# Performance work log

Measured on AMD Instinct MI355X. Metric: run time of the kernel, lower is better.

Reference implementation:

```python
import jax, jax.numpy as jnp
import numpy as np

NUM_CLASSES = 100


def setup_inputs() -> dict:
    key = jax.random.key(0)
    k1, k2, k3, k4 = jax.random.split(key, 4)
    x = jax.random.normal(k1, (256, 2048), dtype=jnp.float32)
    W_model = jax.random.normal(k2, (2048, 64), dtype=jnp.float32)
    database_code = jax.random.normal(k3, (100000, 64), dtype=jnp.float32)
    database_labels = jax.random.randint(k4, (100000,), 0, NUM_CLASSES, dtype=jnp.int64)
    return {
        "x": x,
        "W_model": W_model,
        "database_code": database_code,
        "database_labels": database_labels,
        "K": 1000,
    }


def reference(x, W_model, database_code, database_labels, K):
    # model(x): single linear projection to hash-code space [B, d]
    out = x @ W_model
    # sim_score = out @ codes.T * -0.5 + num_classes/2  -> [B, N]
    sim = jnp.matmul(out, database_code.T) * -0.5 + NUM_CLASSES / 2
    # np.argpartition(sim, K)[:, :K] selects the K SMALLEST scores.
    # Equivalent set via top_k on negated scores.
    _, topk_idx = jax.lax.top_k(-sim, K)            # [B, K]
    topk_labels = database_labels[topk_idx]          # [B, K]
    # per-class histogram over the top-K retrieved labels
    classes = jnp.arange(NUM_CLASSES, dtype=topk_labels.dtype)
    counts = (topk_labels[:, :, None] == classes[None, None, :]).sum(axis=1)  # [B, C]
    probs = counts.astype(jnp.float32) / K
    return probs
```

## Files before the change

kernel.cpp:

```cpp
#include <hip/hip_runtime.h>
#include <hip/hip_fp16.h>


#define NBK 256
#define FNB 1024
#define CAPC 2048
#define BCAP 2048
#define MROWS 32
#define NCHX 64
#define NCLS 100

typedef _Float16 half8 __attribute__((ext_vector_type(8)));
typedef float floatx4 __attribute__((ext_vector_type(4)));

static __device__ __forceinline__ unsigned packh2(float a, float b) {
  _Float16 ha = (_Float16)a, hb = (_Float16)b;
  unsigned short ua, ub;
  __builtin_memcpy(&ua, &ha, 2); __builtin_memcpy(&ub, &hb, 2);
  return (unsigned)ua | ((unsigned)ub << 16);
}

static __device__ __forceinline__ void rowRange(double b1sq, double cmax,
                                                double& lo, double& inv, double& bw) {
  double hr = 0.5 * sqrt(b1sq * cmax) * 1.000001 + 9.0;
  lo = 50.0 - hr;
  bw = (2.0 * hr) / (double)NBK;
  inv = (double)NBK / (2.0 * hr);
}

static __device__ __forceinline__ void loadA(const unsigned short* __restrict__ out16,
                                             int m0, int mr, int quad,
                                             half8& a00, half8& a01, half8& a10, half8& a11) {
  const uint4* o4 = (const uint4*)out16;
  uint4 u;
  u = o4[(size_t)(m0 + mr) * 8 + quad];          __builtin_memcpy(&a00, &u, 16);
  u = o4[(size_t)(m0 + mr) * 8 + 4 + quad];      __builtin_memcpy(&a01, &u, 16);
  u = o4[(size_t)(m0 + 16 + mr) * 8 + quad];     __builtin_memcpy(&a10, &u, 16);
  u = o4[(size_t)(m0 + 16 + mr) * 8 + 4 + quad]; __builtin_memcpy(&a11, &u, 16);
}

static __device__ __forceinline__ float reduceCmax256(const float* __restrict__ slab,
                                                      int n, float* fred) {
  int tid = (int)threadIdx.x;
  float m = 0.0f;
  for (int i = tid; i < n; i += 256) m = fmaxf(m, slab[i]);
  fred[tid] = m; __syncthreads();
  for (int off = 128; off > 0; off >>= 1) {
    if (tid < off) fred[tid] = fmaxf(fred[tid], fred[tid + off]);
    __syncthreads();
  }
  float r = fred[0];
  __syncthreads();
  return r;
}

__global__ __launch_bounds__(1024) void k_prep(const float* __restrict__ x,
                                               const float* __restrict__ W,
                                               const float* __restrict__ codes,
                                               const int* __restrict__ labels,
                                               int N, int Npad, int D, int B, int nCvt,
                                               unsigned short* __restrict__ codes16,
                                               float* __restrict__ cmaxSlab,
                                               double* __restrict__ out64,
                                               unsigned short* __restrict__ out16,
                                               double* __restrict__ B1sq,
                                               int* __restrict__ shiftp) {
  __shared__ double red[1024];
  __shared__ float xs[2048];
  __shared__ float fredw[16];
  __shared__ int flag;
  int blk = (int)blockIdx.x, tid = (int)threadIdx.x;
  int lane = tid & 63, wid = tid >> 6;
  if (blk < nCvt) {
    int gl = tid & 15, g = tid >> 4;
    int base = blk * 256;
    int r0 = base + g, r1 = base + 64 + g, r2 = base + 128 + g, r3 = base + 192 + g;
    float4 q0 = {0.f,0.f,0.f,0.f}, q1 = q0, q2 = q0, q3 = q0;
    if (r0 < N) q0 = ((const float4*)(codes + (size_t)r0 * 64))[gl];
    if (r1 < N) q1 = ((const float4*)(codes + (size_t)r1 * 64))[gl];
    if (r2 < N) q2 = ((const float4*)(codes + (size_t)r2 * 64))[gl];
    if (r3 < N) q3 = ((const float4*)(codes + (size_t)r3 * 64))[gl];
    uint2 o0, o1, o2, o3;
    o0.x = packh2(q0.x, q0.y); o0.y = packh2(q0.z, q0.w);
    o1.x = packh2(q1.x, q1.y); o1.y = packh2(q1.z, q1.w);
    o2.x = packh2(q2.x, q2.y); o2.y = packh2(q2.z, q2.w);
    o3.x = packh2(q3.x, q3.y); o3.y = packh2(q3.z, q3.w);
    ((uint2*)(codes16 + (size_t)r0 * 64))[gl] = o0;
    ((uint2*)(codes16 + (size_t)r1 * 64))[gl] = o1;
    ((uint2*)(codes16 + (size_t)r2 * 64))[gl] = o2;
    ((uint2*)(codes16 + (size_t)r3 * 64))[gl] = o3;
    float bmax = 0.0f;
#define NRM(qv)                                                            \
    { double c2 = fma((double)(qv).x, (double)(qv).x, 0.0);                \
      c2 = fma((double)(qv).y, (double)(qv).y, c2);                        \
      c2 = fma((double)(qv).z, (double)(qv).z, c2);                        \
      c2 = fma((double)(qv).w, (double)(qv).w, c2);                        \
      c2 += __shfl_xor(c2, 1, 16); c2 += __shfl_xor(c2, 2, 16);            \
      c2 += __shfl_xor(c2, 4, 16); c2 += __shfl_xor(c2, 8, 16);            \
      bmax = fmaxf(bmax, (float)(c2 * 1.000001)); }
    NRM(q0) NRM(q1) NRM(q2) NRM(q3)
#undef NRM
#pragma unroll
    for (int off = 32; off > 0; off >>= 1) bmax = fmaxf(bmax, __shfl_xor(bmax, off, 64));
    if (lane == 0) fredw[wid] = bmax;
    __syncthreads();
    if (tid == 0) {
      float m = fredw[0];
#pragma unroll
      for (int j = 1; j < 16; ++j) m = fmaxf(m, fredw[j]);
      cmaxSlab[blk] = m;
    }
  } else if (blk < nCvt + B) {
    int b = blk - nCvt;
    const float* xr = x + (size_t)b * D;
    for (int i = tid; i < (D >> 1); i += 1024)
      ((float2*)xs)[i] = ((const float2*)xr)[i];
    __syncthreads();
    int t = tid & 63, w = tid >> 6;
    int kc = D >> 4;
    int k0 = w * kc;
    double a[8];
#pragma unroll
    for (int j = 0; j < 8; ++j) a[j] = 0.0;
#pragma unroll 2
    for (int k = k0; k < k0 + kc; k += 8) {
#pragma unroll
      for (int j = 0; j < 8; ++j)
        a[j] = fma((double)xs[k + j], (double)W[(size_t)(k + j) * 64 + t], a[j]);
    }
    red[tid] = ((a[0] + a[1]) + (a[2] + a[3])) + ((a[4] + a[5]) + (a[6] + a[7]));
    __syncthreads();
    if (w == 0) {
      double o = 0.0;
#pragma unroll
      for (int j = 0; j < 16; ++j) o += red[t + 64 * j];
      out64[(size_t)b * 64 + t] = o;
      _Float16 h = (_Float16)(float)o;
      unsigned short us; __builtin_memcpy(&us, &h, 2);
      out16[(size_t)b * 64 + t] = us;
      double sq = o * o;
#pragma unroll
      for (int off = 1; off < 64; off <<= 1) sq += __shfl_xor(sq, off, 64);
      if (t == 0) B1sq[b] = sq;
    }
  } else {
    if (tid == 0) flag = 0;
    __syncthreads();
    int m = N < 256 ? N : 256;
    if (tid < m && labels[2 * tid + 1] != 0) atomicOr(&flag, 1);
    __syncthreads();
    if (tid == 0) *shiftp = flag ? 0 : 1;
  }
}

__global__ __launch_bounds__(256) void k_mhist(const unsigned short* __restrict__ codes16,
                                               const unsigned short* __restrict__ out16,
                                               const double* __restrict__ B1sq,
                                               const float* __restrict__ cmaxSlab,
                                               int nCvt, int N, int Npad, int cpb, int B,
                                               unsigned short* __restrict__ histg,
                                               unsigned char* __restrict__ buck) {
  __shared__ unsigned hist[MROWS * NBK];
  __shared__ float sP[MROWS], sQ[MROWS], fred[256];
  int tid = (int)threadIdx.x;
  int m0 = (int)blockIdx.y * MROWS, cx = (int)blockIdx.x;
  float cmax = reduceCmax256(cmaxSlab, nCvt, fred);
  for (int i = tid; i < MROWS * NBK; i += 256) hist[i] = 0u;
  if (tid < MROWS) {
    double lo, inv, bw;
    rowRange(B1sq[m0 + tid], (double)cmax, lo, inv, bw);
    sP[tid] = (float)(-0.5 * inv);
    sQ[tid] = (float)((50.0 - lo) * inv);
  }
  __syncthreads();
  int l = tid & 63, w = tid >> 6;
  int quad = l >> 4, mr = l & 15;
  half8 a00, a01, a10, a11;
  loadA(out16, m0, mr, quad, a00, a01, a10, a11);
  float P0[4], Q0[4], P1[4], Q1[4];
#pragma unroll
  for (int r = 0; r < 4; ++r) {
    P0[r] = sP[quad*4 + r];      Q0[r] = sQ[quad*4 + r];
    P1[r] = sP[16 + quad*4 + r]; Q1[r] = sQ[16 + quad*4 + r];
  }
  int cstart = cx * cpb;
  int cend = cstart + cpb; if (cend > N) cend = N;
  const uint4* c4 = (const uint4*)codes16;
  floatx4 z = {0.f, 0.f, 0.f, 0.f};
  for (int base = cstart; base < cend; base += 64) {
    int nrow = base + w * 16 + mr;
    int nc = nrow < Npad ? nrow : Npad - 1;
    uint4 ub0 = c4[(size_t)nc * 8 + quad];
    uint4 ub1 = c4[(size_t)nc * 8 + 4 + quad];
    half8 b0, b1;
    __builtin_memcpy(&b0, &ub0, 16); __builtin_memcpy(&b1, &ub1, 16);
    floatx4 d0 = __builtin_amdgcn_mfma_f32_16x16x32_f16(a00, b0, z, 0, 0, 0);
    d0 = __builtin_amdgcn_mfma_f32_16x16x32_f16(a01, b1, d0, 0, 0, 0);
    floatx4 d1 = __builtin_amdgcn_mfma_f32_16x16x32_f16(a10, b0, z, 0, 0, 0);
    d1 = __builtin_amdgcn_mfma_f32_16x16x32_f16(a11, b1, d1, 0, 0, 0);
    if (nrow < N) {
#pragma unroll
      for (int r = 0; r < 4; ++r) {
        int bk0 = (int)fmaf(d0[r], P0[r], Q0[r]);
        bk0 = bk0 < 0 ? 0 : (bk0 > NBK-1 ? NBK-1 : bk0);
        atomicAdd(&hist[(quad*4 + r) * NBK + bk0], 1u);
        buck[(size_t)(m0 + quad*4 + r) * N + nrow] = (unsigned char)bk0;
        int bk1 = (int)fmaf(d1[r], P1[r], Q1[r]);
        bk1 = bk1 < 0 ? 0 : (bk1 > NBK-1 ? NBK-1 : bk1);
        atomicAdd(&hist[(16 + quad*4 + r) * NBK + bk1], 1u);
        buck[(size_t)(m0 + 16 + quad*4 + r) * N + nrow] = (unsigned char)bk1;
      }
    }
  }
  __syncthreads();
  for (int i = tid; i < MROWS * NBK; i += 256)
    histg[((size_t)cx * B + (m0 + (i >> 8))) * NBK + (i & (NBK - 1))] =
        (unsigned short)hist[i];
}

__global__ __launch_bounds__(1024) void k_rowfinal(const float* __restrict__ codes,
                                                   const double* __restrict__ out64,
                                                   const double* __restrict__ B1sq,
                                                   const float* __restrict__ cmaxSlab,
                                                   const unsigned short* __restrict__ histg,
                                                   const unsigned char* __restrict__ buck,
                                                   const int* __restrict__ labels,
                                                   const int* __restrict__ shiftp,
                                                   const int* __restrict__ Kp,
                                                   float* __restrict__ outp,
                                                   int nCvt, int N, int B) {
  __shared__ float fredw[16];
  __shared__ unsigned sp[1024];
  __shared__ unsigned s[NBK];
  __shared__ unsigned wtot[4];
  __shared__ double key[CAPC];
  __shared__ int kidx[CAPC];
  __shared__ int blist[BCAP];
  __shared__ unsigned fhist[FNB];
  __shared__ unsigned ftot[16];
  __shared__ unsigned short tlist[CAPC];
  __shared__ double sod[64];
  __shared__ unsigned lab[NCLS];
  __shared__ unsigned ccnt, bcnt, tcnt, sCntLt;
  __shared__ int sTb, sFtb;
  int b = (int)blockIdx.x, tid = (int)threadIdx.x;
  int lane = tid & 63, wid = tid >> 6;

  {
    float m = (tid < nCvt) ? cmaxSlab[tid] : 0.0f;
    for (int i = tid + 1024; i < nCvt; i += 1024) m = fmaxf(m, cmaxSlab[i]);
#pragma unroll
    for (int off = 32; off > 0; off >>= 1) m = fmaxf(m, __shfl_xor(m, off, 64));
    if (lane == 0) fredw[wid] = m;
  }
  fhist[tid] = 0u;
  if (tid < 64) sod[tid] = out64[(size_t)b * 64 + tid];
  if (tid < NCLS) lab[tid] = 0u;
  if (tid == 0) { ccnt = 0u; bcnt = 0u; tcnt = 0u; sCntLt = 0u; sFtb = FNB; }
  __syncthreads();
  float cmax;
  { float m = fredw[0];
#pragma unroll
    for (int j = 1; j < 16; ++j) m = fmaxf(m, fredw[j]);
    cmax = m; }

  {
    int bk = tid & 255, cq = tid >> 8;
    unsigned part = 0;
#pragma unroll
    for (int t2 = 0; t2 < 16; ++t2)
      part += (unsigned)histg[((size_t)(cq * 16 + t2) * B + b) * NBK + bk];
    sp[tid] = part;
  }
  __syncthreads();
  {
    unsigned v = 0;
    if (tid < 256) {
      v = sp[tid] + sp[tid + 256] + sp[tid + 512] + sp[tid + 768];
#pragma unroll
      for (int off = 1; off < 64; off <<= 1) {
        unsigned t = (unsigned)__shfl_up((int)v, off, 64);
        if (lane >= off) v += t;
      }
      if (lane == 63) wtot[wid] = v;
    }
    __syncthreads();
    if (tid < 256) {
      for (int j = 0; j < wid; ++j) v += wtot[j];
      s[tid] = v;
    }
  }
  __syncthreads();
  unsigned K = (unsigned)Kp[0];
  if (tid < 256) {
    unsigned prev = tid ? s[tid - 1] : 0u;
    if (s[tid] >= K && prev < K) sTb = tid;
  }
  __syncthreads();
  int tb = sTb;
  double lo, inv, bwd;
  rowRange(B1sq[b], (double)cmax, lo, inv, bwd);
  double S = sqrt(B1sq[b] * (double)cmax);
  double Mtot = 2.0 * (0.5 * S * 1.1e-3 + 0.05) + 1e-3;
  int q = (int)ceil(Mtot / bwd);
  int belowMax = tb - 1 - q;
  int candMax = tb + 1 + q;
  if (candMax > NBK - 1) candMax = NBK - 1;
  unsigned btot = (belowMax >= 0) ? s[belowMax] : 0u;
  int shift = *shiftp;

  {
    const uint4* bw16 = (const uint4*)(buck + (size_t)b * N);
    int nw16 = N >> 4;
#define CLS1(nn, bkv)                                                  \
    { int bk_ = (int)(bkv);                                            \
      if (bk_ <= belowMax) {                                           \
        unsigned p_ = atomicAdd(&bcnt, 1u);                            \
        if (p_ < BCAP) blist[p_] = (nn);                               \
      } else if (bk_ <= candMax) {                                     \
        unsigned p_ = atomicAdd(&ccnt, 1u);                            \
        if (p_ < CAPC) kidx[p_] = (nn);                                \
      } }
#define PROCV(vv, nb)                                                  \
    { unsigned w_;                                                     \
      w_ = (vv).x; CLS1((nb)+0,  w_ & 0xFF) CLS1((nb)+1,  (w_>>8)&0xFF)\
                   CLS1((nb)+2,  (w_>>16)&0xFF) CLS1((nb)+3,  w_>>24)  \
      w_ = (vv).y; CLS1((nb)+4,  w_ & 0xFF) CLS1((nb)+5,  (w_>>8)&0xFF)\
                   CLS1((nb)+6,  (w_>>16)&0xFF) CLS1((nb)+7,  w_>>24)  \
      w_ = (vv).z; CLS1((nb)+8,  w_ & 0xFF) CLS1((nb)+9,  (w_>>8)&0xFF)\
                   CLS1((nb)+10, (w_>>16)&0xFF) CLS1((nb)+11, w_>>24)  \
      w_ = (vv).w; CLS1((nb)+12, w_ & 0xFF) CLS1((nb)+13, (w_>>8)&0xFF)\
                   CLS1((nb)+14, (w_>>16)&0xFF) CLS1((nb)+15, w_>>24) }
    for (int i = tid; i < nw16; i += 2048) {
      uint4 v0 = bw16[i];
      int i1 = i + 1024; bool h1 = i1 < nw16;
      uint4 v1 = {0u, 0u, 0u, 0u};
      if (h1) v1 = bw16[i1];
      PROCV(v0, i << 4)
      if (h1) PROCV(v1, i1 << 4)
    }
#undef PROCV
    for (int n = (nw16 << 4) + tid; n < N; n += 1024) {
      CLS1(n, buck[(size_t)b * N + n])
    }
#undef CLS1
  }
  __syncthreads();

  {
    int bm = (int)bcnt; if (bm > BCAP) bm = BCAP;
    for (int i = tid; i < bm; i += 1024)
      atomicAdd(&lab[labels[(size_t)blist[i] << shift]], 1u);
  }
  int cc = (int)ccnt; if (cc > CAPC) cc = CAPC;
  {
    int g = tid >> 4, gl = tid & 15;
    for (int i = g; i < cc; i += 64) {
      int n = kidx[i];
      float4 qv = ((const float4*)(codes + (size_t)n * 64))[gl];
      double p = fma((double)qv.x, sod[gl*4+0], 0.0);
      p = fma((double)qv.y, sod[gl*4+1], p);
      p = fma((double)qv.z, sod[gl*4+2], p);
      p = fma((double)qv.w, sod[gl*4+3], p);
      p += __shfl_xor(p, 1, 16);
      p += __shfl_xor(p, 2, 16);
      p += __shfl_xor(p, 4, 16);
      p += __shfl_xor(p, 8, 16);
      if (gl == 0) key[i] = fma(p, -0.5, 50.0);
    }
  }
  __syncthreads();

  int need = (int)K - (int)btot;
  double fLo = lo + (double)(belowMax + 1) * bwd - Mtot;
  double fInv = (double)FNB / ((double)(candMax - belowMax) * bwd + 2.0 * Mtot);
  for (int i = tid; i < cc; i += 1024) {
    int fb = (int)((key[i] - fLo) * fInv);
    fb = fb < 0 ? 0 : (fb > FNB - 1 ? FNB - 1 : fb);
    atomicAdd(&fhist[fb], 1u);
  }
  __syncthreads();
  {
    unsigned v = fhist[tid];
#pragma unroll
    for (int off = 1; off < 64; off <<= 1) {
      unsigned t = (unsigned)__shfl_up((int)v, off, 64);
      if (lane >= off) v += t;
    }
    if (lane == 63) ftot[wid] = v;
    sp[tid] = v;
  }
  __syncthreads();
  {
    unsigned off = 0;
    for (int j = 0; j < wid; ++j) off += ftot[j];
    unsigned ci = sp[tid] + off;
    unsigned ce = ci - fhist[tid];
    if ((int)ci >= need && (int)ce < need) { sFtb = tid; sCntLt = ce; }
  }
  __syncthreads();
  int ftb = sFtb;
  for (int i = tid; i < cc; i += 1024) {
    int fb = (int)((key[i] - fLo) * fInv);
    fb = fb < 0 ? 0 : (fb > FNB - 1 ? FNB - 1 : fb);
    if (fb < ftb) {
      atomicAdd(&lab[labels[(size_t)kidx[i] << shift]], 1u);
    } else if (fb == ftb) {
      unsigned p_ = atomicAdd(&tcnt, 1u);
      if (p_ < CAPC) tlist[p_] = (unsigned short)i;
    }
  }
  __syncthreads();
  {
    int tn = (int)tcnt; if (tn > CAPC) tn = CAPC;
    int rem = need - (int)sCntLt;
    for (int j = tid; j < tn; j += 1024) {
      int i = (int)tlist[j];
      double ki = key[i]; int ii = kidx[i];
      int rank = 0;
      for (int j2 = 0; j2 < tn; ++j2) {
        int i2 = (int)tlist[j2];
        double k2 = key[i2];
        rank += (k2 < ki || (k2 == ki && kidx[i2] < ii)) ? 1 : 0;
      }
      if (rank < rem) atomicAdd(&lab[labels[(size_t)ii << shift]], 1u);
    }
  }
  __syncthreads();
  double Kd = (double)K;
  for (int c = tid; c < NCLS; c += 1024)
    outp[b * NCLS + c] = (float)((double)lab[c] / Kd);
}

extern "C" void kernel_launch(void* const* d_in, const int* in_sizes, int n_in,
                              void* d_out, int out_size, void* d_ws, size_t ws_size,
                              hipStream_t stream) {
  const float* x     = (const float*)d_in[0];
  const float* W     = (const float*)d_in[1];
  const float* codes = (const float*)d_in[2];
  const int* labels  = (const int*)d_in[3];
  const int* Kp      = (const int*)d_in[4];

  const int B = out_size / NCLS;
  const int N = in_sizes[3];
  const int D = in_sizes[0] / B;
  const int Npad = (N + 255) & ~255;
  const int cpb = (((N + NCHX - 1) / NCHX) + 63) & ~63;
  const int nCvt = Npad / 256;

  char* p = (char*)d_ws;
  double* out64      = (double*)p;   p += (size_t)B * 64 * sizeof(double);
  unsigned short* out16 = (unsigned short*)p; p += (size_t)B * 64 * 2;
  double* B1sq       = (double*)p;   p += (size_t)B * sizeof(double);
  int* shiftp        = (int*)p;      p += 64;
  float* cmaxSlab    = (float*)p;    p += 4096;
  unsigned short* histg = (unsigned short*)p; p += (size_t)NCHX * B * NBK * 2;
  unsigned char* buck   = (unsigned char*)p;  p += (size_t)B * N;
  unsigned short* codes16 = (unsigned short*)p;

  k_prep<<<nCvt + B + 1, 1024, 0, stream>>>(x, W, codes, labels, N, Npad, D, B, nCvt,
                                            codes16, cmaxSlab, out64, out16, B1sq, shiftp);
  k_mhist<<<dim3(NCHX, B / MROWS), 256, 0, stream>>>(codes16, out16, B1sq, cmaxSlab,
                                                     nCvt, N, Npad, cpb, B, histg, buck);
  k_rowfinal<<<B, 1024, 0, stream>>>(codes, out64, B1sq, cmaxSlab, histg, buck,
                                     labels, shiftp, Kp, (float*)d_out, nCvt, N, B);
}
```

Measured before the change: 152.4 us.

## Coalesce bucket stores via LDS tile, per-wave candidate lists, SWAR byte prefilter

k_mhist now handles 16 rows per block instead of 32. Bucket bytes are staged in a double-buffered shared tile and written out as coalesced 4-byte stores instead of scattered byte stores. k_rowfinal replaces the global shared counters with per-wave segment counters and lists, then compacts them, to cut atomic contention. A SWAR byte test skips 4-byte words whose buckets all exceed candMax. Per-wave caps of 256 could overflow or drop entries where the old global caps did not, and halving MROWS doubles the grid and the code reads per block.

After: 158.0 us. +3.6%, slower.

```diff
diff --git a/kernel.cpp b/kernel.cpp
--- a/kernel.cpp
+++ b/kernel.cpp
@@ -5,8 +5,8 @@
 #define NBK 256
 #define FNB 1024
 #define CAPC 2048
-#define BCAP 2048
-#define MROWS 32
+#define SEGC 256
+#define MROWS 16
 #define NCHX 64
 #define NCLS 100
 
@@ -26,17 +26,6 @@
   lo = 50.0 - hr;
   bw = (2.0 * hr) / (double)NBK;
   inv = (double)NBK / (2.0 * hr);
-}
-
-static __device__ __forceinline__ void loadA(const unsigned short* __restrict__ out16,
-                                             int m0, int mr, int quad,
-                                             half8& a00, half8& a01, half8& a10, half8& a11) {
-  const uint4* o4 = (const uint4*)out16;
-  uint4 u;
-  u = o4[(size_t)(m0 + mr) * 8 + quad];          __builtin_memcpy(&a00, &u, 16);
-  u = o4[(size_t)(m0 + mr) * 8 + 4 + quad];      __builtin_memcpy(&a01, &u, 16);
-  u = o4[(size_t)(m0 + 16 + mr) * 8 + quad];     __builtin_memcpy(&a10, &u, 16);
-  u = o4[(size_t)(m0 + 16 + mr) * 8 + 4 + quad]; __builtin_memcpy(&a11, &u, 16);
 }
 
 static __device__ __forceinline__ float reduceCmax256(const float* __restrict__ slab,
@@ -161,6 +150,7 @@
                                                unsigned short* __restrict__ histg,
                                                unsigned char* __restrict__ buck) {
   __shared__ unsigned hist[MROWS * NBK];
+  __shared__ unsigned char tile[2][MROWS * 64];
   __shared__ float sP[MROWS], sQ[MROWS], fred[256];
   int tid = (int)threadIdx.x;
   int m0 = (int)blockIdx.y * MROWS, cx = (int)blockIdx.x;
@@ -175,18 +165,22 @@
   __syncthreads();
   int l = tid & 63, w = tid >> 6;
   int quad = l >> 4, mr = l & 15;
-  half8 a00, a01, a10, a11;
-  loadA(out16, m0, mr, quad, a00, a01, a10, a11);
-  float P0[4], Q0[4], P1[4], Q1[4];
-#pragma unroll
-  for (int r = 0; r < 4; ++r) {
-    P0[r] = sP[quad*4 + r];      Q0[r] = sQ[quad*4 + r];
-    P1[r] = sP[16 + quad*4 + r]; Q1[r] = sQ[16 + quad*4 + r];
-  }
+  half8 a00, a01;
+  {
+    const uint4* o4 = (const uint4*)out16;
+    uint4 u;
+    u = o4[(size_t)(m0 + mr) * 8 + quad];     __builtin_memcpy(&a00, &u, 16);
+    u = o4[(size_t)(m0 + mr) * 8 + 4 + quad]; __builtin_memcpy(&a01, &u, 16);
+  }
+  float P0[4], Q0[4];
+#pragma unroll
+  for (int r = 0; r < 4; ++r) { P0[r] = sP[quad*4 + r]; Q0[r] = sQ[quad*4 + r]; }
   int cstart = cx * cpb;
   int cend = cstart + cpb; if (cend > N) cend = N;
   const uint4* c4 = (const uint4*)codes16;
   floatx4 z = {0.f, 0.f, 0.f, 0.f};
+  int buf = 0;
+  int srow = tid >> 4, spart = tid & 15;
   for (int base = cstart; base < cend; base += 64) {
     int nrow = base + w * 16 + mr;
     int nc = nrow < Npad ? nrow : Npad - 1;
@@ -196,21 +190,26 @@
     __builtin_memcpy(&b0, &ub0, 16); __builtin_memcpy(&b1, &ub1, 16);
     floatx4 d0 = __builtin_amdgcn_mfma_f32_16x16x32_f16(a00, b0, z, 0, 0, 0);
     d0 = __builtin_amdgcn_mfma_f32_16x16x32_f16(a01, b1, d0, 0, 0, 0);
-    floatx4 d1 = __builtin_amdgcn_mfma_f32_16x16x32_f16(a10, b0, z, 0, 0, 0);
-    d1 = __builtin_amdgcn_mfma_f32_16x16x32_f16(a11, b1, d1, 0, 0, 0);
-    if (nrow < N) {
-#pragma unroll
-      for (int r = 0; r < 4; ++r) {
-        int bk0 = (int)fmaf(d0[r], P0[r], Q0[r]);
-        bk0 = bk0 < 0 ? 0 : (bk0 > NBK-1 ? NBK-1 : bk0);
-        atomicAdd(&hist[(quad*4 + r) * NBK + bk0], 1u);
-        buck[(size_t)(m0 + quad*4 + r) * N + nrow] = (unsigned char)bk0;
-        int bk1 = (int)fmaf(d1[r], P1[r], Q1[r]);
-        bk1 = bk1 < 0 ? 0 : (bk1 > NBK-1 ? NBK-1 : bk1);
-        atomicAdd(&hist[(16 + quad*4 + r) * NBK + bk1], 1u);
-        buck[(size_t)(m0 + 16 + quad*4 + r) * N + nrow] = (unsigned char)bk1;
+#pragma unroll
+    for (int r = 0; r < 4; ++r) {
+      int bk0 = (int)fmaf(d0[r], P0[r], Q0[r]);
+      bk0 = bk0 < 0 ? 0 : (bk0 > NBK-1 ? NBK-1 : bk0);
+      if (nrow < N) atomicAdd(&hist[(quad*4 + r) * NBK + bk0], 1u);
+      tile[buf][(quad*4 + r) * 64 + w * 16 + mr] = (unsigned char)bk0;
+    }
+    __syncthreads();
+    {
+      int n0 = base + spart * 4;
+      unsigned v = ((const unsigned*)tile[buf])[(srow << 4) + spart];
+      unsigned char* dst = buck + (size_t)(m0 + srow) * N + n0;
+      if (n0 + 3 < N) *(unsigned*)dst = v;
+      else {
+#pragma unroll
+        for (int k2 = 0; k2 < 4; ++k2)
+          if (n0 + k2 < N) dst[k2] = (unsigned char)(v >> (8 * k2));
       }
     }
+    buf ^= 1;
   }
   __syncthreads();
   for (int i = tid; i < MROWS * NBK; i += 256)
@@ -235,13 +234,16 @@
   __shared__ unsigned wtot[4];
   __shared__ double key[CAPC];
   __shared__ int kidx[CAPC];
-  __shared__ int blist[BCAP];
+  __shared__ int kidxS[16 * SEGC];
+  __shared__ int blistS[16 * SEGC];
+  __shared__ unsigned bcntS[16], ccntS[16];
+  __shared__ int coff[17], cCopy[16];
   __shared__ unsigned fhist[FNB];
   __shared__ unsigned ftot[16];
   __shared__ unsigned short tlist[CAPC];
   __shared__ double sod[64];
   __shared__ unsigned lab[NCLS];
-  __shared__ unsigned ccnt, bcnt, tcnt, sCntLt;
+  __shared__ unsigned tcnt, sCntLt;
   __shared__ int sTb, sFtb;
   int b = (int)blockIdx.x, tid = (int)threadIdx.x;
   int lane = tid & 63, wid = tid >> 6;
@@ -256,7 +258,8 @@
   fhist[tid] = 0u;
   if (tid < 64) sod[tid] = out64[(size_t)b * 64 + tid];
   if (tid < NCLS) lab[tid] = 0u;
-  if (tid == 0) { ccnt = 0u; bcnt = 0u; tcnt = 0u; sCntLt = 0u; sFtb = FNB; }
+  if (tid < 16) { bcntS[tid] = 0u; ccntS[tid] = 0u; }
+  if (tid == 0) { tcnt = 0u; sCntLt = 0u; sFtb = FNB; }
   __syncthreads();
   float cmax;
   { float m = fredw[0];
@@ -312,47 +315,65 @@
   {
     const uint4* bw16 = (const uint4*)(buck + (size_t)b * N);
     int nw16 = N >> 4;
-#define CLS1(nn, bkv)                                                  \
-    { int bk_ = (int)(bkv);                                            \
-      if (bk_ <= belowMax) {                                           \
-        unsigned p_ = atomicAdd(&bcnt, 1u);                            \
-        if (p_ < BCAP) blist[p_] = (nn);                               \
-      } else if (bk_ <= candMax) {                                     \
-        unsigned p_ = atomicAdd(&ccnt, 1u);                            \
-        if (p_ < CAPC) kidx[p_] = (nn);                                \
+    bool fast = (candMax <= 127);
+    unsigned c1x = (unsigned)(candMax + 1) * 0x01010101u;
+#define CLSB(nn, bv)                                                       \
+    { int bk_ = (int)(bv);                                                 \
+      if (bk_ <= belowMax) {                                               \
+        unsigned p_ = atomicAdd(&bcntS[wid], 1u);                          \
+        if (p_ < SEGC) blistS[(wid << 8) + p_] = (nn);                     \
+      } else if (bk_ <= candMax) {                                         \
+        unsigned p_ = atomicAdd(&ccntS[wid], 1u);                          \
+        if (p_ < SEGC) kidxS[(wid << 8) + p_] = (nn);                      \
       } }
-#define PROCV(vv, nb)                                                  \
-    { unsigned w_;                                                     \
-      w_ = (vv).x; CLS1((nb)+0,  w_ & 0xFF) CLS1((nb)+1,  (w_>>8)&0xFF)\
-                   CLS1((nb)+2,  (w_>>16)&0xFF) CLS1((nb)+3,  w_>>24)  \
-      w_ = (vv).y; CLS1((nb)+4,  w_ & 0xFF) CLS1((nb)+5,  (w_>>8)&0xFF)\
-                   CLS1((nb)+6,  (w_>>16)&0xFF) CLS1((nb)+7,  w_>>24)  \
-      w_ = (vv).z; CLS1((nb)+8,  w_ & 0xFF) CLS1((nb)+9,  (w_>>8)&0xFF)\
-                   CLS1((nb)+10, (w_>>16)&0xFF) CLS1((nb)+11, w_>>24)  \
-      w_ = (vv).w; CLS1((nb)+12, w_ & 0xFF) CLS1((nb)+13, (w_>>8)&0xFF)\
-                   CLS1((nb)+14, (w_>>16)&0xFF) CLS1((nb)+15, w_>>24) }
+#define PROCW(w_, nb)                                                      \
+    if (!fast || (((w_) - c1x) & ~(w_) & 0x80808080u)) {                   \
+      CLSB((nb)+0, (w_) & 0xFF)        CLSB((nb)+1, ((w_) >> 8) & 0xFF)    \
+      CLSB((nb)+2, ((w_) >> 16) & 0xFF) CLSB((nb)+3, (w_) >> 24)           \
+    }
     for (int i = tid; i < nw16; i += 2048) {
       uint4 v0 = bw16[i];
       int i1 = i + 1024; bool h1 = i1 < nw16;
       uint4 v1 = {0u, 0u, 0u, 0u};
       if (h1) v1 = bw16[i1];
-      PROCV(v0, i << 4)
-      if (h1) PROCV(v1, i1 << 4)
-    }
-#undef PROCV
+      int nb0 = i << 4;
+      PROCW(v0.x, nb0) PROCW(v0.y, nb0 + 4) PROCW(v0.z, nb0 + 8) PROCW(v0.w, nb0 + 12)
+      if (h1) {
+        int nb1 = i1 << 4;
+        PROCW(v1.x, nb1) PROCW(v1.y, nb1 + 4) PROCW(v1.z, nb1 + 8) PROCW(v1.w, nb1 + 12)
+      }
+    }
+#undef PROCW
     for (int n = (nw16 << 4) + tid; n < N; n += 1024) {
-      CLS1(n, buck[(size_t)b * N + n])
-    }
-#undef CLS1
-  }
-  __syncthreads();
-
-  {
-    int bm = (int)bcnt; if (bm > BCAP) bm = BCAP;
-    for (int i = tid; i < bm; i += 1024)
-      atomicAdd(&lab[labels[(size_t)blist[i] << shift]], 1u);
-  }
-  int cc = (int)ccnt; if (cc > CAPC) cc = CAPC;
+      CLSB(n, buck[(size_t)b * N + n])
+    }
+#undef CLSB
+  }
+  __syncthreads();
+
+  if (tid == 0) {
+    int acc = 0;
+    for (int s2 = 0; s2 < 16; ++s2) {
+      coff[s2] = acc;
+      int c = (int)ccntS[s2]; if (c > SEGC) c = SEGC;
+      if (acc + c > CAPC) c = CAPC - acc;
+      cCopy[s2] = c; acc += c;
+    }
+    coff[16] = acc;
+  }
+  __syncthreads();
+  for (int i = tid; i < 16 * SEGC; i += 1024) {
+    int s2 = i >> 8, j = i & (SEGC - 1);
+    if (j < cCopy[s2]) kidx[coff[s2] + j] = kidxS[i];
+  }
+  for (int i = tid; i < 16 * SEGC; i += 1024) {
+    int s2 = i >> 8, j = i & (SEGC - 1);
+    unsigned bc = bcntS[s2]; if (bc > SEGC) bc = SEGC;
+    if ((unsigned)j < bc)
+      atomicAdd(&lab[labels[(size_t)blistS[i] << shift]], 1u);
+  }
+  __syncthreads();
+  int cc = coff[16];
   {
     int g = tid >> 4, gl = tid & 15;
     for (int i = g; i < cc; i += 64) {
```

## Widen histogram blocks to 512 threads and add SWAR byte-skip in row scan

Applied to the files above, without the earlier changes.

The histogram kernel now runs 8 waves per block, each covering 128 database rows per iteration. The cmax reduction becomes wave shuffles plus a single shared-memory step, replacing a tree of barriers. In the per-row classification scan, a SWAR test skips any 4-byte word in which no bucket is at or below candMax, cutting per-byte branching. In exchange there are more LDS atomics contending per block, and the skip path only applies when candMax is 127 or less.

Result: no change. 152.7 us (+0.2%).

```diff
diff --git a/kernel.cpp b/kernel.cpp
--- a/kernel.cpp
+++ b/kernel.cpp
@@ -37,21 +37,6 @@
   u = o4[(size_t)(m0 + mr) * 8 + 4 + quad];      __builtin_memcpy(&a01, &u, 16);
   u = o4[(size_t)(m0 + 16 + mr) * 8 + quad];     __builtin_memcpy(&a10, &u, 16);
   u = o4[(size_t)(m0 + 16 + mr) * 8 + 4 + quad]; __builtin_memcpy(&a11, &u, 16);
-}
-
-static __device__ __forceinline__ float reduceCmax256(const float* __restrict__ slab,
-                                                      int n, float* fred) {
-  int tid = (int)threadIdx.x;
-  float m = 0.0f;
-  for (int i = tid; i < n; i += 256) m = fmaxf(m, slab[i]);
-  fred[tid] = m; __syncthreads();
-  for (int off = 128; off > 0; off >>= 1) {
-    if (tid < off) fred[tid] = fmaxf(fred[tid], fred[tid + off]);
-    __syncthreads();
-  }
-  float r = fred[0];
-  __syncthreads();
-  return r;
 }
 
 __global__ __launch_bounds__(1024) void k_prep(const float* __restrict__ x,
@@ -153,7 +138,7 @@
   }
 }
 
-__global__ __launch_bounds__(256) void k_mhist(const unsigned short* __restrict__ codes16,
+__global__ __launch_bounds__(512) void k_mhist(const unsigned short* __restrict__ codes16,
                                                const unsigned short* __restrict__ out16,
                                                const double* __restrict__ B1sq,
                                                const float* __restrict__ cmaxSlab,
@@ -161,11 +146,24 @@
                                                unsigned short* __restrict__ histg,
                                                unsigned char* __restrict__ buck) {
   __shared__ unsigned hist[MROWS * NBK];
-  __shared__ float sP[MROWS], sQ[MROWS], fred[256];
+  __shared__ float sP[MROWS], sQ[MROWS], fredw[8];
   int tid = (int)threadIdx.x;
+  int lane = tid & 63, wv = tid >> 6;
   int m0 = (int)blockIdx.y * MROWS, cx = (int)blockIdx.x;
-  float cmax = reduceCmax256(cmaxSlab, nCvt, fred);
-  for (int i = tid; i < MROWS * NBK; i += 256) hist[i] = 0u;
+  {
+    float m = 0.0f;
+    for (int i = tid; i < nCvt; i += 512) m = fmaxf(m, cmaxSlab[i]);
+#pragma unroll
+    for (int off = 32; off > 0; off >>= 1) m = fmaxf(m, __shfl_xor(m, off, 64));
+    if (lane == 0) fredw[wv] = m;
+  }
+  for (int i = tid; i < MROWS * NBK; i += 512) hist[i] = 0u;
+  __syncthreads();
+  float cmax;
+  { float m = fredw[0];
+#pragma unroll
+    for (int j = 1; j < 8; ++j) m = fmaxf(m, fredw[j]);
+    cmax = m; }
   if (tid < MROWS) {
     double lo, inv, bw;
     rowRange(B1sq[m0 + tid], (double)cmax, lo, inv, bw);
@@ -173,8 +171,7 @@
     sQ[tid] = (float)((50.0 - lo) * inv);
   }
   __syncthreads();
-  int l = tid & 63, w = tid >> 6;
-  int quad = l >> 4, mr = l & 15;
+  int quad = lane >> 4, mr = lane & 15;
   half8 a00, a01, a10, a11;
   loadA(out16, m0, mr, quad, a00, a01, a10, a11);
   float P0[4], Q0[4], P1[4], Q1[4];
@@ -187,8 +184,8 @@
   int cend = cstart + cpb; if (cend > N) cend = N;
   const uint4* c4 = (const uint4*)codes16;
   floatx4 z = {0.f, 0.f, 0.f, 0.f};
-  for (int base = cstart; base < cend; base += 64) {
-    int nrow = base + w * 16 + mr;
+  for (int base = cstart; base < cend; base += 128) {
+    int nrow = base + wv * 16 + mr;
     int nc = nrow < Npad ? nrow : Npad - 1;
     uint4 ub0 = c4[(size_t)nc * 8 + quad];
     uint4 ub1 = c4[(size_t)nc * 8 + 4 + quad];
@@ -213,7 +210,7 @@
     }
   }
   __syncthreads();
-  for (int i = tid; i < MROWS * NBK; i += 256)
+  for (int i = tid; i < MROWS * NBK; i += 512)
     histg[((size_t)cx * B + (m0 + (i >> 8))) * NBK + (i & (NBK - 1))] =
         (unsigned short)hist[i];
 }
@@ -312,6 +309,8 @@
   {
     const uint4* bw16 = (const uint4*)(buck + (size_t)b * N);
     int nw16 = N >> 4;
+    bool fast = (candMax <= 127);
+    unsigned c1x = (unsigned)(candMax + 1) * 0x01010101u;
 #define CLS1(nn, bkv)                                                  \
     { int bk_ = (int)(bkv);                                            \
       if (bk_ <= belowMax) {                                           \
@@ -321,25 +320,24 @@
         unsigned p_ = atomicAdd(&ccnt, 1u);                            \
         if (p_ < CAPC) kidx[p_] = (nn);                                \
       } }
-#define PROCV(vv, nb)                                                  \
-    { unsigned w_;                                                     \
-      w_ = (vv).x; CLS1((nb)+0,  w_ & 0xFF) CLS1((nb)+1,  (w_>>8)&0xFF)\
-                   CLS1((nb)+2,  (w_>>16)&0xFF) CLS1((nb)+3,  w_>>24)  \
-      w_ = (vv).y; CLS1((nb)+4,  w_ & 0xFF) CLS1((nb)+5,  (w_>>8)&0xFF)\
-                   CLS1((nb)+6,  (w_>>16)&0xFF) CLS1((nb)+7,  w_>>24)  \
-      w_ = (vv).z; CLS1((nb)+8,  w_ & 0xFF) CLS1((nb)+9,  (w_>>8)&0xFF)\
-                   CLS1((nb)+10, (w_>>16)&0xFF) CLS1((nb)+11, w_>>24)  \
-      w_ = (vv).w; CLS1((nb)+12, w_ & 0xFF) CLS1((nb)+13, (w_>>8)&0xFF)\
-                   CLS1((nb)+14, (w_>>16)&0xFF) CLS1((nb)+15, w_>>24) }
+#define PROCW(w_, nb)                                                  \
+    if (!fast || (((w_) - c1x) & ~(w_) & 0x80808080u)) {               \
+      CLS1((nb)+0, (w_) & 0xFF)         CLS1((nb)+1, ((w_) >> 8) & 0xFF) \
+      CLS1((nb)+2, ((w_) >> 16) & 0xFF) CLS1((nb)+3, (w_) >> 24)       \
+    }
     for (int i = tid; i < nw16; i += 2048) {
       uint4 v0 = bw16[i];
       int i1 = i + 1024; bool h1 = i1 < nw16;
       uint4 v1 = {0u, 0u, 0u, 0u};
       if (h1) v1 = bw16[i1];
-      PROCV(v0, i << 4)
-      if (h1) PROCV(v1, i1 << 4)
-    }
-#undef PROCV
+      int nb0 = i << 4;
+      PROCW(v0.x, nb0) PROCW(v0.y, nb0 + 4) PROCW(v0.z, nb0 + 8) PROCW(v0.w, nb0 + 12)
+      if (h1) {
+        int nb1 = i1 << 4;
+        PROCW(v1.x, nb1) PROCW(v1.y, nb1 + 4) PROCW(v1.z, nb1 + 8) PROCW(v1.w, nb1 + 12)
+      }
+    }
+#undef PROCW
     for (int n = (nw16 << 4) + tid; n < N; n += 1024) {
       CLS1(n, buck[(size_t)b * N + n])
     }
@@ -445,7 +443,7 @@
   const int N = in_sizes[3];
   const int D = in_sizes[0] / B;
   const int Npad = (N + 255) & ~255;
-  const int cpb = (((N + NCHX - 1) / NCHX) + 63) & ~63;
+  const int cpb = (((N + NCHX - 1) / NCHX) + 127) & ~127;
   const int nCvt = Npad / 256;
 
   char* p = (char*)d_ws;
@@ -460,7 +458,7 @@
 
   k_prep<<<nCvt + B + 1, 1024, 0, stream>>>(x, W, codes, labels, N, Npad, D, B, nCvt,
                                             codes16, cmaxSlab, out64, out16, B1sq, shiftp);
-  k_mhist<<<dim3(NCHX, B / MROWS), 256, 0, stream>>>(codes16, out16, B1sq, cmaxSlab,
+  k_mhist<<<dim3(NCHX, B / MROWS), 512, 0, stream>>>(codes16, out16, B1sq, cmaxSlab,
                                                      nCvt, N, Npad, cpb, B, histg, buck);
   k_rowfinal<<<B, 1024, 0, stream>>>(codes, out64, B1sq, cmaxSlab, histg, buck,
                                      labels, shiftp, Kp, (float*)d_out, nCvt, N, B);
```
